# Kernel optimization log

Measured on AMD Instinct MI355X. Metric: run time of the kernel, lower is better.

## Reference

```python
import jax, jax.numpy as jnp
import numpy as np

ALPHA = 3.0
NITERS = 15
POWER_ITERS = 20
ROOTS = [np.cos(np.pi * (2 * i + 1) / (2 * NITERS)) for i in range(NITERS)]


def batch_conv2d(inputs, kernels):
    # inputs: [B,1,H,W], kernels: [B,1,3,3]; per-sample 3x3 stencil via grouped conv
    B, _, H, W = inputs.shape
    out = jax.lax.conv_general_dilated(
        inputs.reshape(1, B, H, W), kernels,
        window_strides=(1, 1), padding=((1, 1), (1, 1)),
        feature_group_count=B,
        dimension_numbers=("NCHW", "OIHW", "NCHW"))
    return out.reshape(B, 1, H, W)


def setup_inputs() -> dict:
    key = jax.random.key(0)
    k1, k2, k3, k4 = jax.random.split(key, 4)
    B, H, W = 64, 512, 512
    x = jax.random.normal(k1, (B, 1, H, W), dtype=jnp.float32)
    f = jax.random.normal(k2, (B, 1, H, W), dtype=jnp.float32)
    kernelA = jax.random.normal(k3, (B, 1, 3, 3), dtype=jnp.float32)
    u = jax.random.normal(k4, (B, 1, H, W), dtype=jnp.float32)
    return {"x": x, "f": f, "kernelA": kernelA, "u": u}


def reference(x, f, kernelA, u):
    # Power iteration to estimate the dominant eigenvalue magnitude m per sample
    for _ in range(POWER_ITERS):
        y = batch_conv2d(u, kernelA)
        m = jnp.max(jnp.abs(y), axis=(2, 3), keepdims=True)  # [B,1,1,1]
        u = y / m
    # Chebyshev step sizes over the band [m/alpha, m]
    taus = jnp.stack(
        [2.0 / (m + m / ALPHA - (m / ALPHA - m) * r) for r in ROOTS])  # [niters,B,1,1,1]

    def cheby_step(xc, tau):
        Ax = batch_conv2d(xc, kernelA)
        return xc + tau * (f - Ax), None

    x, _ = jax.lax.scan(cheby_step, x, taus)
    return x
```

## Files before the change

kernel.cpp:

```cpp
#include <hip/hip_runtime.h>

#define BB 64
#define HH 512
#define WW 512
#define PLANE (HH * WW)
#define R 64
#define NSTRIPE (HH / R)
#define N_CHEBY 15

struct Sl { float a, b, c, d; };

__device__ __forceinline__ void racc(const Sl& s, float k0, float k1, float k2,
                                     float& o0, float& o1) {
    o0 = fmaf(k0, s.a, fmaf(k1, s.b, fmaf(k2, s.c, o0)));
    o1 = fmaf(k0, s.b, fmaf(k1, s.c, fmaf(k2, s.d, o1)));
}

__device__ __forceinline__ Sl ldsl(const float* pl, int row, int c2, bool ok) {
    Sl s = {0.f, 0.f, 0.f, 0.f};
    if (ok) {
        const float* rp = pl + (size_t)row * WW;
        float2 v = *reinterpret_cast<const float2*>(rp + c2);
        s.b = v.x; s.c = v.y;
        if (c2 > 0)      s.a = rp[c2 - 1];
        if (c2 + 2 < WW) s.d = rp[c2 + 2];
    }
    return s;
}

__device__ __forceinline__ void softbar() {
    __asm__ volatile("s_waitcnt lgkmcnt(0)" ::: "memory");
    __builtin_amdgcn_s_barrier();
}

template<int FDv>
__global__ __launch_bounds__(256, 2) void conv_fusedN(
    const float* __restrict__ in, const float* __restrict__ kern,
    const float* __restrict__ pm_prev, float* __restrict__ out,
    float* __restrict__ pmw, float* __restrict__ pmz)
{
    const int b = blockIdx.y, stripe = blockIdx.x, ytop = stripe * R;
    const int t = threadIdx.x, c2 = t << 1;

    __shared__ float re[FDv - 1][2][258], ro[FDv - 1][2][258];
    __shared__ float sred[8];
    __shared__ float sinv;

    if (t < 2 * (FDv - 1)) {
        const int l = t >> 1, par = t & 1;
        re[l][par][0] = 0.f; re[l][par][257] = 0.f;
        ro[l][par][0] = 0.f; ro[l][par][257] = 0.f;
    }
    if (pm_prev && t < 64) {
        float v = (t < NSTRIPE) ? pm_prev[b * NSTRIPE + t] : 0.f;
#pragma unroll
        for (int o = 8; o; o >>= 1) v = fmaxf(v, __shfl_xor(v, o, 64));
        if (t == 0) sinv = 1.f / v;
    }
    __syncthreads();
    const float invv = pm_prev ? sinv : 1.f;

    const float* kb = kern + b * 9;
    const float k00=kb[0],k01=kb[1],k02=kb[2],k10=kb[3],k11=kb[4],k12=kb[5],
                k20=kb[6],k21=kb[7],k22=kb[8];
    const float* ip = in + (size_t)b * PLANE;
    float* op = out ? out + (size_t)b * PLANE : nullptr;

    Sl u2 = {0,0,0,0}, u1 = {0,0,0,0};
    Sl ltp[FDv - 1], lmd[FDv - 1];
    float own0[FDv - 1], own1[FDv - 1];
#pragma unroll
    for (int l = 0; l < FDv - 1; ++l) {
        ltp[l] = Sl{0,0,0,0}; lmd[l] = Sl{0,0,0,0};
        own0[l] = 0.f; own1[l] = 0.f;
    }
    float mz = 0.f, mw = 0.f;
    Sl u0 = ldsl(ip, ytop - FDv, c2, (unsigned)(ytop - FDv) < HH);

    const int STEPS   = R + 3 * FDv - 1;
    const int LOADCUT = R + 2 * FDv - 1;
#pragma unroll 2
    for (int p = 0; p < STEPS; ++p) {
        const int yu = ytop - FDv + p;
        Sl un = ldsl(ip, yu + 1, c2, ((unsigned)(yu + 1) < HH) && (p < LOADCUT));

        const int rpar = (p + 1) & 1, wpar = p & 1;
        Sl am[FDv - 1];
#pragma unroll
        for (int l = 0; l < FDv - 1; ++l) {
            am[l].a = ro[l][rpar][t];
            am[l].b = own0[l];
            am[l].c = own1[l];
            am[l].d = re[l][rpar][2 + t];
        }

        float v0[FDv], v1[FDv];
        {
            float s0 = 0.f, s1 = 0.f;
            racc(u2, k00,k01,k02, s0,s1);
            racc(u1, k10,k11,k12, s0,s1);
            racc(u0, k20,k21,k22, s0,s1);
            const int y = yu - 1;
            const bool act = (y >= ytop - (FDv-1)) && (y <= ytop + R + FDv - 2)
                          && ((unsigned)y < HH);
            v0[0] = act ? s0 * invv : 0.f;
            v1[0] = act ? s1 * invv : 0.f;
        }
#pragma unroll
        for (int j = 2; j <= FDv; ++j) {
            float s0 = 0.f, s1 = 0.f;
            racc(ltp[j-2], k00,k01,k02, s0,s1);
            racc(lmd[j-2], k10,k11,k12, s0,s1);
            racc(am[j-2],  k20,k21,k22, s0,s1);
            const int y = yu - (2*j - 1);
            if (j < FDv) {
                const bool act = (y >= ytop - (FDv-j)) && (y <= ytop + R + FDv - j - 1)
                              && ((unsigned)y < HH);
                v0[j-1] = act ? s0 : 0.f;
                v1[j-1] = act ? s1 : 0.f;
                if (j == FDv - 1)
                    mz = fmaxf(mz, fmaxf(fabsf(v0[j-1]), fabsf(v1[j-1])));
            } else {
                if (y >= ytop && y < ytop + R) {
                    mw = fmaxf(mw, fmaxf(fabsf(s0), fabsf(s1)));
                    if (op)
                        *reinterpret_cast<float2*>(op + (size_t)y * WW + c2) =
                            make_float2(s0, s1);
                }
            }
        }
#pragma unroll
        for (int l = 0; l < FDv - 1; ++l) {
            re[l][wpar][1 + t] = v0[l];
            ro[l][wpar][1 + t] = v1[l];
            ltp[l] = lmd[l]; lmd[l] = am[l];
            own0[l] = v0[l]; own1[l] = v1[l];
        }
        u2 = u1; u1 = u0; u0 = un;
        softbar();
    }

#pragma unroll
    for (int o = 32; o; o >>= 1) {
        mz = fmaxf(mz, __shfl_xor(mz, o, 64));
        mw = fmaxf(mw, __shfl_xor(mw, o, 64));
    }
    if ((t & 63) == 0) { sred[t >> 6] = mz; sred[4 + (t >> 6)] = mw; }
    __syncthreads();
    if (t == 0) {
        pmz[b * NSTRIPE + stripe] =
            fmaxf(fmaxf(sred[0], sred[1]), fmaxf(sred[2], sred[3]));
        pmw[b * NSTRIPE + stripe] =
            fmaxf(fmaxf(sred[4], sred[5]), fmaxf(sred[6], sred[7]));
    }
}

__global__ __launch_bounds__(64) void tau_fused(
    const float* __restrict__ pmz, const float* __restrict__ pmw,
    float* __restrict__ taus)
{
    const int b = blockIdx.x, t = threadIdx.x;
    float vz = (t < NSTRIPE) ? pmz[b * NSTRIPE + t] : 0.f;
    float vw = (t < NSTRIPE) ? pmw[b * NSTRIPE + t] : 0.f;
#pragma unroll
    for (int o = 8; o; o >>= 1) {
        vz = fmaxf(vz, __shfl_xor(vz, o, 64));
        vw = fmaxf(vw, __shfl_xor(vw, o, 64));
    }
    if (t < N_CHEBY) {
        const float m = vw / vz;
        const double rr = cos(M_PI * (2.0 * t + 1.0) / (2.0 * N_CHEBY));
        const float denom = m + m / 3.0f - (m / 3.0f - m) * (float)rr;
        taus[t * BB + b] = 2.0f / denom;
    }
}

template<int FDv>
__global__ __launch_bounds__(256, 2) void cheby_fusedN(
    const float* __restrict__ xin, const float* __restrict__ fin,
    const float* __restrict__ kern, const float* __restrict__ tauv,
    float* __restrict__ xout)
{
    const int b = blockIdx.y, stripe = blockIdx.x, ytop = stripe * R;
    const int t = threadIdx.x, c2 = t << 1;

    __shared__ float re[FDv - 1][2][258], ro[FDv - 1][2][258];

    if (t < 2 * (FDv - 1)) {
        const int l = t >> 1, par = t & 1;
        re[l][par][0] = 0.f; re[l][par][257] = 0.f;
        ro[l][par][0] = 0.f; ro[l][par][257] = 0.f;
    }
    __syncthreads();

    const float* kb = kern + b * 9;
    const float k00=kb[0],k01=kb[1],k02=kb[2],k10=kb[3],k11=kb[4],k12=kb[5],
                k20=kb[6],k21=kb[7],k22=kb[8];
    float tau[FDv];
#pragma unroll
    for (int j = 0; j < FDv; ++j) tau[j] = tauv[j * BB + b];

    const float* xp = xin + (size_t)b * PLANE;
    const float* fp = fin + (size_t)b * PLANE;
    float* op = xout + (size_t)b * PLANE;

    Sl u2 = {0,0,0,0}, u1 = {0,0,0,0};
    Sl ltp[FDv - 1], lmd[FDv - 1];
    float own0[FDv - 1], own1[FDv - 1];
#pragma unroll
    for (int l = 0; l < FDv - 1; ++l) {
        ltp[l] = Sl{0,0,0,0}; lmd[l] = Sl{0,0,0,0};
        own0[l] = 0.f; own1[l] = 0.f;
    }
    float2 fh[2 * FDv - 1];
#pragma unroll
    for (int k = 1; k < 2 * FDv - 1; ++k) fh[k] = make_float2(0.f, 0.f);

    Sl u0 = ldsl(xp, ytop - FDv, c2, (unsigned)(ytop - FDv) < HH);
    {
        const int yf = ytop - FDv - 1;
        fh[0] = ((unsigned)yf < HH)
            ? *reinterpret_cast<const float2*>(fp + (size_t)yf * WW + c2)
            : make_float2(0.f, 0.f);
    }

    const int STEPS   = R + 3 * FDv - 1;
    const int LOADCUT = R + 2 * FDv - 1;
#pragma unroll 2
    for (int p = 0; p < STEPS; ++p) {
        const int yu = ytop - FDv + p;
        const bool ldok = (p < LOADCUT);
        Sl un = ldsl(xp, yu + 1, c2, ((unsigned)(yu + 1) < HH) && ldok);
        const float2 fn = (((unsigned)yu < HH) && ldok)
            ? *reinterpret_cast<const float2*>(fp + (size_t)yu * WW + c2)
            : make_float2(0.f, 0.f);

        const int rpar = (p + 1) & 1, wpar = p & 1;
        Sl am[FDv - 1];
#pragma unroll
        for (int l = 0; l < FDv - 1; ++l) {
            am[l].a = ro[l][rpar][t];
            am[l].b = own0[l];
            am[l].c = own1[l];
            am[l].d = re[l][rpar][2 + t];
        }

        float v0[FDv], v1[FDv];
        {
            float s0 = 0.f, s1 = 0.f;
            racc(u2, k00,k01,k02, s0,s1);
            racc(u1, k10,k11,k12, s0,s1);
            racc(u0, k20,k21,k22, s0,s1);
            const int y = yu - 1;
            const bool act = (y >= ytop - (FDv-1)) && (y <= ytop + R + FDv - 2)
                          && ((unsigned)y < HH);
            v0[0] = act ? fmaf(tau[0], fh[0].x - s0, u1.b) : 0.f;
            v1[0] = act ? fmaf(tau[0], fh[0].y - s1, u1.c) : 0.f;
        }
#pragma unroll
        for (int j = 2; j <= FDv; ++j) {
            float s0 = 0.f, s1 = 0.f;
            racc(ltp[j-2], k00,k01,k02, s0,s1);
            racc(lmd[j-2], k10,k11,k12, s0,s1);
            racc(am[j-2],  k20,k21,k22, s0,s1);
            const int y = yu - (2*j - 1);
            const float2 fv = fh[2*(j-1)];
            if (j < FDv) {
                const bool act = (y >= ytop - (FDv-j)) && (y <= ytop + R + FDv - j - 1)
                              && ((unsigned)y < HH);
                v0[j-1] = act ? fmaf(tau[j-1], fv.x - s0, lmd[j-2].b) : 0.f;
                v1[j-1] = act ? fmaf(tau[j-1], fv.y - s1, lmd[j-2].c) : 0.f;
            } else {
                if (y >= ytop && y < ytop + R) {
                    const float o0 = fmaf(tau[FDv-1], fv.x - s0, lmd[j-2].b);
                    const float o1 = fmaf(tau[FDv-1], fv.y - s1, lmd[j-2].c);
                    *reinterpret_cast<float2*>(op + (size_t)y * WW + c2) =
                        make_float2(o0, o1);
                }
            }
        }
#pragma unroll
        for (int l = 0; l < FDv - 1; ++l) {
            re[l][wpar][1 + t] = v0[l];
            ro[l][wpar][1 + t] = v1[l];
            ltp[l] = lmd[l]; lmd[l] = am[l];
            own0[l] = v0[l]; own1[l] = v1[l];
        }
        u2 = u1; u1 = u0; u0 = un;
#pragma unroll
        for (int k = 2 * FDv - 2; k > 0; --k) fh[k] = fh[k - 1];
        fh[0] = fn;
        softbar();
    }
}

extern "C" void kernel_launch(void* const* d_in, const int* in_sizes, int n_in,
                              void* d_out, int out_size, void* d_ws, size_t ws_size,
                              hipStream_t stream)
{
    const float* x_in = (const float*)d_in[0];
    const float* f_in = (const float*)d_in[1];
    const float* k_in = (const float*)d_in[2];
    const float* u_in = (const float*)d_in[3];
    float* out = (float*)d_out;

    float* bufA = (float*)d_ws;
    float* pmW0 = bufA + (size_t)BB * PLANE;
    float* pmW1 = pmW0 + BB * NSTRIPE;
    float* pmZ  = pmW1 + BB * NSTRIPE;
    float* taus = pmZ  + BB * NSTRIPE;

    dim3 blk(256), grd(NSTRIPE, BB);

    conv_fusedN<10><<<grd, blk, 0, stream>>>(u_in, k_in, nullptr, bufA, pmW0, pmZ);
    conv_fusedN<10><<<grd, blk, 0, stream>>>(bufA, k_in, pmW0, nullptr, pmW1, pmZ);

    tau_fused<<<BB, 64, 0, stream>>>(pmZ, pmW1, taus);

    cheby_fusedN<8><<<grd, blk, 0, stream>>>(x_in, f_in, k_in, taus, bufA);
    cheby_fusedN<7><<<grd, blk, 0, stream>>>(bufA, f_in, k_in, taus + 8 * BB, out);
}
```

Baseline: 391.4 us.

## Split Chebyshev into three 5-step passes with smaller stripes and reloaded f

```diff
diff --git a/kernel.cpp b/kernel.cpp
--- a/kernel.cpp
+++ b/kernel.cpp
@@ -4,8 +4,6 @@
 #define HH 512
 #define WW 512
 #define PLANE (HH * WW)
-#define R 64
-#define NSTRIPE (HH / R)
 #define N_CHEBY 15
 
 struct Sl { float a, b, c, d; };
@@ -33,13 +31,14 @@
     __builtin_amdgcn_s_barrier();
 }
 
-template<int FDv>
+template<int FDv, int RR>
 __global__ __launch_bounds__(256, 2) void conv_fusedN(
     const float* __restrict__ in, const float* __restrict__ kern,
     const float* __restrict__ pm_prev, float* __restrict__ out,
     float* __restrict__ pmw, float* __restrict__ pmz)
 {
-    const int b = blockIdx.y, stripe = blockIdx.x, ytop = stripe * R;
+    constexpr int NS = HH / RR;
+    const int b = blockIdx.y, stripe = blockIdx.x, ytop = stripe * RR;
     const int t = threadIdx.x, c2 = t << 1;
 
     __shared__ float re[FDv - 1][2][258], ro[FDv - 1][2][258];
@@ -52,7 +51,7 @@
         ro[l][par][0] = 0.f; ro[l][par][257] = 0.f;
     }
     if (pm_prev && t < 64) {
-        float v = (t < NSTRIPE) ? pm_prev[b * NSTRIPE + t] : 0.f;
+        float v = (t < NS) ? pm_prev[b * NS + t] : 0.f;
 #pragma unroll
         for (int o = 8; o; o >>= 1) v = fmaxf(v, __shfl_xor(v, o, 64));
         if (t == 0) sinv = 1.f / v;
@@ -77,8 +76,8 @@
     float mz = 0.f, mw = 0.f;
     Sl u0 = ldsl(ip, ytop - FDv, c2, (unsigned)(ytop - FDv) < HH);
 
-    const int STEPS   = R + 3 * FDv - 1;
-    const int LOADCUT = R + 2 * FDv - 1;
+    const int STEPS   = RR + 3 * FDv - 1;
+    const int LOADCUT = RR + 2 * FDv - 1;
 #pragma unroll 2
     for (int p = 0; p < STEPS; ++p) {
         const int yu = ytop - FDv + p;
@@ -101,7 +100,7 @@
             racc(u1, k10,k11,k12, s0,s1);
             racc(u0, k20,k21,k22, s0,s1);
             const int y = yu - 1;
-            const bool act = (y >= ytop - (FDv-1)) && (y <= ytop + R + FDv - 2)
+            const bool act = (y >= ytop - (FDv-1)) && (y <= ytop + RR + FDv - 2)
                           && ((unsigned)y < HH);
             v0[0] = act ? s0 * invv : 0.f;
             v1[0] = act ? s1 * invv : 0.f;
@@ -114,14 +113,14 @@
             racc(am[j-2],  k20,k21,k22, s0,s1);
             const int y = yu - (2*j - 1);
             if (j < FDv) {
-                const bool act = (y >= ytop - (FDv-j)) && (y <= ytop + R + FDv - j - 1)
+                const bool act = (y >= ytop - (FDv-j)) && (y <= ytop + RR + FDv - j - 1)
                               && ((unsigned)y < HH);
                 v0[j-1] = act ? s0 : 0.f;
                 v1[j-1] = act ? s1 : 0.f;
                 if (j == FDv - 1)
                     mz = fmaxf(mz, fmaxf(fabsf(v0[j-1]), fabsf(v1[j-1])));
             } else {
-                if (y >= ytop && y < ytop + R) {
+                if (y >= ytop && y < ytop + RR) {
                     mw = fmaxf(mw, fmaxf(fabsf(s0), fabsf(s1)));
                     if (op)
                         *reinterpret_cast<float2*>(op + (size_t)y * WW + c2) =
@@ -148,9 +147,9 @@
     if ((t & 63) == 0) { sred[t >> 6] = mz; sred[4 + (t >> 6)] = mw; }
     __syncthreads();
     if (t == 0) {
-        pmz[b * NSTRIPE + stripe] =
+        pmz[b * NS + stripe] =
             fmaxf(fmaxf(sred[0], sred[1]), fmaxf(sred[2], sred[3]));
-        pmw[b * NSTRIPE + stripe] =
+        pmw[b * NS + stripe] =
             fmaxf(fmaxf(sred[4], sred[5]), fmaxf(sred[6], sred[7]));
     }
 }
@@ -159,9 +158,10 @@
     const float* __restrict__ pmz, const float* __restrict__ pmw,
     float* __restrict__ taus)
 {
+    constexpr int NS = 8;
     const int b = blockIdx.x, t = threadIdx.x;
-    float vz = (t < NSTRIPE) ? pmz[b * NSTRIPE + t] : 0.f;
-    float vw = (t < NSTRIPE) ? pmw[b * NSTRIPE + t] : 0.f;
+    float vz = (t < NS) ? pmz[b * NS + t] : 0.f;
+    float vw = (t < NS) ? pmw[b * NS + t] : 0.f;
 #pragma unroll
     for (int o = 8; o; o >>= 1) {
         vz = fmaxf(vz, __shfl_xor(vz, o, 64));
@@ -176,20 +176,24 @@
 }
 
 template<int FDv>
-__global__ __launch_bounds__(256, 2) void cheby_fusedN(
+__global__ __launch_bounds__(256, 4) void cheby9(
     const float* __restrict__ xin, const float* __restrict__ fin,
     const float* __restrict__ kern, const float* __restrict__ tauv,
     float* __restrict__ xout)
 {
-    const int b = blockIdx.y, stripe = blockIdx.x, ytop = stripe * R;
+    constexpr int RR = 32, NS = HH / RR;
+    constexpr int STEPS   = RR + 3 * FDv - 1;
+    constexpr int LOADCUT = RR + 2 * FDv - 1;
+    constexpr int FILLEND = 3 * FDv - 4;
+
+    const int b = blockIdx.y, stripe = blockIdx.x, ytop = stripe * RR;
     const int t = threadIdx.x, c2 = t << 1;
 
-    __shared__ float re[FDv - 1][2][258], ro[FDv - 1][2][258];
-
+    __shared__ float2 rc[FDv - 1][2][258];
     if (t < 2 * (FDv - 1)) {
         const int l = t >> 1, par = t & 1;
-        re[l][par][0] = 0.f; re[l][par][257] = 0.f;
-        ro[l][par][0] = 0.f; ro[l][par][257] = 0.f;
+        rc[l][par][0]   = make_float2(0.f, 0.f);
+        rc[l][par][257] = make_float2(0.f, 0.f);
     }
     __syncthreads();
 
@@ -212,50 +216,61 @@
         ltp[l] = Sl{0,0,0,0}; lmd[l] = Sl{0,0,0,0};
         own0[l] = 0.f; own1[l] = 0.f;
     }
-    float2 fh[2 * FDv - 1];
-#pragma unroll
-    for (int k = 1; k < 2 * FDv - 1; ++k) fh[k] = make_float2(0.f, 0.f);
 
     Sl u0 = ldsl(xp, ytop - FDv, c2, (unsigned)(ytop - FDv) < HH);
+    float2 fcur = make_float2(0.f, 0.f);
     {
         const int yf = ytop - FDv - 1;
-        fh[0] = ((unsigned)yf < HH)
-            ? *reinterpret_cast<const float2*>(fp + (size_t)yf * WW + c2)
-            : make_float2(0.f, 0.f);
-    }
-
-    const int STEPS   = R + 3 * FDv - 1;
-    const int LOADCUT = R + 2 * FDv - 1;
-#pragma unroll 2
-    for (int p = 0; p < STEPS; ++p) {
+        if ((unsigned)yf < HH)
+            fcur = *reinterpret_cast<const float2*>(fp + (size_t)yf * WW + c2);
+    }
+
+    auto step = [&](const int p, const bool MASKED)
+        __attribute__((always_inline))
+    {
         const int yu = ytop - FDv + p;
         const bool ldok = (p < LOADCUT);
-        Sl un = ldsl(xp, yu + 1, c2, ((unsigned)(yu + 1) < HH) && ldok);
-        const float2 fn = (((unsigned)yu < HH) && ldok)
-            ? *reinterpret_cast<const float2*>(fp + (size_t)yu * WW + c2)
-            : make_float2(0.f, 0.f);
+        Sl un = ldsl(xp, yu + 1, c2, ldok && (!MASKED || (unsigned)(yu + 1) < HH));
+        float2 fn = make_float2(0.f, 0.f);
+        if (ldok && (!MASKED || (unsigned)yu < HH))
+            fn = *reinterpret_cast<const float2*>(fp + (size_t)yu * WW + c2);
+
+        float2 fj[FDv - 1];
+#pragma unroll
+        for (int j = 2; j <= FDv; ++j) {
+            const int yf = yu - (2 * j - 1);
+            fj[j - 2] = make_float2(0.f, 0.f);
+            if (!MASKED || (unsigned)yf < HH)
+                fj[j - 2] = *reinterpret_cast<const float2*>(fp + (size_t)yf * WW + c2);
+        }
 
         const int rpar = (p + 1) & 1, wpar = p & 1;
         Sl am[FDv - 1];
 #pragma unroll
         for (int l = 0; l < FDv - 1; ++l) {
-            am[l].a = ro[l][rpar][t];
+            const float* F = reinterpret_cast<const float*>(&rc[l][rpar][0]);
+            am[l].a = F[2 * t + 1];
             am[l].b = own0[l];
             am[l].c = own1[l];
-            am[l].d = re[l][rpar][2 + t];
-        }
-
-        float v0[FDv], v1[FDv];
+            am[l].d = F[2 * t + 4];
+        }
+
+        float v0[FDv - 1], v1[FDv - 1];
         {
             float s0 = 0.f, s1 = 0.f;
             racc(u2, k00,k01,k02, s0,s1);
             racc(u1, k10,k11,k12, s0,s1);
             racc(u0, k20,k21,k22, s0,s1);
-            const int y = yu - 1;
-            const bool act = (y >= ytop - (FDv-1)) && (y <= ytop + R + FDv - 2)
-                          && ((unsigned)y < HH);
-            v0[0] = act ? fmaf(tau[0], fh[0].x - s0, u1.b) : 0.f;
-            v1[0] = act ? fmaf(tau[0], fh[0].y - s1, u1.c) : 0.f;
+            float nv0 = fmaf(tau[0], fcur.x - s0, u1.b);
+            float nv1 = fmaf(tau[0], fcur.y - s1, u1.c);
+            if (MASKED) {
+                const int y = yu - 1;
+                const bool act = (y >= ytop - (FDv-1)) && (y <= ytop + RR + FDv - 2)
+                              && ((unsigned)y < HH);
+                nv0 = act ? nv0 : 0.f;
+                nv1 = act ? nv1 : 0.f;
+            }
+            v0[0] = nv0; v1[0] = nv1;
         }
 #pragma unroll
         for (int j = 2; j <= FDv; ++j) {
@@ -263,15 +278,20 @@
             racc(ltp[j-2], k00,k01,k02, s0,s1);
             racc(lmd[j-2], k10,k11,k12, s0,s1);
             racc(am[j-2],  k20,k21,k22, s0,s1);
-            const int y = yu - (2*j - 1);
-            const float2 fv = fh[2*(j-1)];
+            const int y = yu - (2 * j - 1);
+            const float2 fv = fj[j - 2];
             if (j < FDv) {
-                const bool act = (y >= ytop - (FDv-j)) && (y <= ytop + R + FDv - j - 1)
-                              && ((unsigned)y < HH);
-                v0[j-1] = act ? fmaf(tau[j-1], fv.x - s0, lmd[j-2].b) : 0.f;
-                v1[j-1] = act ? fmaf(tau[j-1], fv.y - s1, lmd[j-2].c) : 0.f;
+                float nv0 = fmaf(tau[j-1], fv.x - s0, lmd[j-2].b);
+                float nv1 = fmaf(tau[j-1], fv.y - s1, lmd[j-2].c);
+                if (MASKED) {
+                    const bool act = (y >= ytop - (FDv-j)) && (y <= ytop + RR + FDv - j - 1)
+                                  && ((unsigned)y < HH);
+                    nv0 = act ? nv0 : 0.f;
+                    nv1 = act ? nv1 : 0.f;
+                }
+                v0[j-1] = nv0; v1[j-1] = nv1;
             } else {
-                if (y >= ytop && y < ytop + R) {
+                if (y >= ytop && y < ytop + RR) {
                     const float o0 = fmaf(tau[FDv-1], fv.x - s0, lmd[j-2].b);
                     const float o1 = fmaf(tau[FDv-1], fv.y - s1, lmd[j-2].c);
                     *reinterpret_cast<float2*>(op + (size_t)y * WW + c2) =
@@ -281,16 +301,25 @@
         }
 #pragma unroll
         for (int l = 0; l < FDv - 1; ++l) {
-            re[l][wpar][1 + t] = v0[l];
-            ro[l][wpar][1 + t] = v1[l];
+            rc[l][wpar][1 + t] = make_float2(v0[l], v1[l]);
             ltp[l] = lmd[l]; lmd[l] = am[l];
             own0[l] = v0[l]; own1[l] = v1[l];
         }
         u2 = u1; u1 = u0; u0 = un;
-#pragma unroll
-        for (int k = 2 * FDv - 2; k > 0; --k) fh[k] = fh[k - 1];
-        fh[0] = fn;
+        fcur = fn;
         softbar();
+    };
+
+    if (stripe == 0 || stripe == NS - 1) {
+#pragma unroll 1
+        for (int p = 0; p < STEPS; ++p) step(p, true);
+    } else {
+#pragma unroll 1
+        for (int p = 0; p < FILLEND; ++p) step(p, true);
+#pragma unroll 2
+        for (int p = FILLEND; p < LOADCUT; ++p) step(p, false);
+#pragma unroll 1
+        for (int p = LOADCUT; p < STEPS; ++p) step(p, true);
     }
 }
 
@@ -306,17 +335,20 @@
 
     float* bufA = (float*)d_ws;
     float* pmW0 = bufA + (size_t)BB * PLANE;
-    float* pmW1 = pmW0 + BB * NSTRIPE;
-    float* pmZ  = pmW1 + BB * NSTRIPE;
-    float* taus = pmZ  + BB * NSTRIPE;
-
-    dim3 blk(256), grd(NSTRIPE, BB);
-
-    conv_fusedN<10><<<grd, blk, 0, stream>>>(u_in, k_in, nullptr, bufA, pmW0, pmZ);
-    conv_fusedN<10><<<grd, blk, 0, stream>>>(bufA, k_in, pmW0, nullptr, pmW1, pmZ);
+    float* pmW1 = pmW0 + BB * 16;
+    float* pmZ  = pmW1 + BB * 16;
+    float* taus = pmZ  + BB * 16;
+
+    dim3 blk(256);
+
+    conv_fusedN<10, 64><<<dim3(8, BB), blk, 0, stream>>>(
+        u_in, k_in, nullptr, bufA, pmW0, pmZ);
+    conv_fusedN<10, 64><<<dim3(8, BB), blk, 0, stream>>>(
+        bufA, k_in, pmW0, nullptr, pmW1, pmZ);
 
     tau_fused<<<BB, 64, 0, stream>>>(pmZ, pmW1, taus);
 
-    cheby_fusedN<8><<<grd, blk, 0, stream>>>(x_in, f_in, k_in, taus, bufA);
-    cheby_fusedN<7><<<grd, blk, 0, stream>>>(bufA, f_in, k_in, taus + 8 * BB, out);
-}
+    cheby9<5><<<dim3(16, BB), blk, 0, stream>>>(x_in, f_in, k_in, taus, out);
+    cheby9<5><<<dim3(16, BB), blk, 0, stream>>>(out,  f_in, k_in, taus + 5 * BB, bufA);
+    cheby9<5><<<dim3(16, BB), blk, 0, stream>>>(bufA, f_in, k_in, taus + 10 * BB, out);
+}
```

Result: slower. 450.3 us (+15.0%).
